# Kernel tuning notes

Measured on AMD Instinct MI355X. Metric: run time of the kernel, lower is better.

The kernel has to match this reference:

```python
import jax, jax.numpy as jnp
import numpy as np

D = 1024      # in_features
H = 4096      # hidden_dims
E = 8         # expert_nums
K = 2         # top_k
B, S = 4, 2048


def setup_inputs() -> dict:
    key = jax.random.key(0)
    ks = jax.random.split(key, 8)
    def lin(k, fan_in, shape):
        bound = 1.0 / np.sqrt(fan_in)
        return jax.random.uniform(k, shape, jnp.float32, -bound, bound)
    return {
        "x":  jax.random.normal(ks[0], (B, S, D), jnp.float32),
        "Wg": lin(ks[1], D, (D, E)),
        "bg": lin(ks[2], D, (E,)),
        "W1": lin(ks[3], D, (E, D, H)),
        "b1": lin(ks[4], D, (E, H)),
        "W2": lin(ks[5], H, (E, H, D)),
        "b2": lin(ks[6], H, (E, D)),
    }


def reference(x, Wg, bg, W1, b1, W2, b2):
    B_, S_, D_ = x.shape
    xt = x.reshape(-1, D_)                                   # [N, D]
    # Router: softmax gating + top-k
    logits = xt @ Wg + bg                                    # [N, E]
    scores = jax.nn.softmax(logits, axis=-1)
    topk_probs, topk_idx = jax.lax.top_k(scores, K)          # [N, K]
    # Dense per-expert FFN (the source runs every expert on all tokens)
    h = jnp.einsum("nd,edh->enh", xt, W1) + b1[:, None, :]   # [E, N, H]
    h = jax.nn.gelu(h, approximate=False)
    eo = jnp.einsum("enh,ehd->end", h, W2) + b2[:, None, :]  # [E, N, D]
    # Gather selected experts per token and combine with gate weights
    eo = jnp.transpose(eo, (1, 0, 2))                        # [N, E, D]
    sel = jnp.take_along_axis(eo, topk_idx[:, :, None], axis=1)  # [N, K, D]
    out = jnp.einsum("nk,nkd->nd", topk_probs, sel)          # [N, D]
    return out.reshape(B_, S_, D_)
```

## Files before the change

### kernel.cpp

```cpp
#include <hip/hip_runtime.h>
#include <hip/hip_bf16.h>
#include <cstdint>
#include <cstddef>

using bf16 = __hip_bfloat16;
using short8 = __attribute__((ext_vector_type(8))) short;
using floatx4 = __attribute__((ext_vector_type(4))) float;

constexpr int D_IN = 1024;
constexpr int H_DIM = 4096;
constexpr int E_NUM = 8;
constexpr int NTOK = 8192;
constexpr int NPAIR = NTOK * 2;

constexpr size_t OFF_PTOK  = 1024;
constexpr size_t OFF_PPROB = 263168;
constexpr size_t OFF_XBF   = 1048576;
constexpr size_t OFF_W2T   = OFF_XBF + (size_t)NTOK * D_IN * 2;
constexpr size_t OFF_HBUF  = OFF_W2T + (size_t)E_NUM * D_IN * H_DIM * 2;
constexpr size_t OFF_W1T   = OFF_HBUF + (size_t)NPAIR * H_DIM * 2;

__device__ __forceinline__ void cp16(const bf16* g, bf16* s) {
  __builtin_amdgcn_global_load_lds(
      (const __attribute__((address_space(1))) unsigned int*)g,
      (__attribute__((address_space(3))) unsigned int*)s, 16, 0, 0);
}

__global__ __launch_bounds__(256) void transpose_cvt(
    const float* __restrict__ in, bf16* __restrict__ out, int K, int N) {
  __shared__ float tile[32][33];
  const int e = blockIdx.z;
  const float* ip = in + (size_t)e * K * N + (size_t)(blockIdx.y * 32) * N + blockIdx.x * 32;
  bf16* op = out + (size_t)e * K * N + (size_t)(blockIdx.x * 32) * K + blockIdx.y * 32;
  const int tx = threadIdx.x & 31, ty = threadIdx.x >> 5;
#pragma unroll
  for (int r = 0; r < 4; r++)
    tile[ty + r * 8][tx] = ip[(size_t)(ty + r * 8) * N + tx];
  __syncthreads();
#pragma unroll
  for (int r = 0; r < 4; r++)
    op[(size_t)(ty + r * 8) * K + tx] = __float2bfloat16(tile[tx][ty + r * 8]);
}

__global__ __launch_bounds__(256) void router_kernel(
    const float* __restrict__ x, const float* __restrict__ Wg,
    const float* __restrict__ bg, bf16* __restrict__ Xbf,
    int* __restrict__ counts, int* __restrict__ pairTok, float* __restrict__ pairProb) {
  const int lane = threadIdx.x & 63;
  const int n = blockIdx.x * 4 + (threadIdx.x >> 6);
  const float* xr = x + (size_t)n * D_IN;
  bf16* xbr = Xbf + (size_t)n * D_IN;
  float logit[E_NUM];
#pragma unroll
  for (int e = 0; e < E_NUM; e++) logit[e] = 0.f;
#pragma unroll
  for (int i = 0; i < 16; i++) {
    const int d = i * 64 + lane;
    const float xd = xr[d];
    xbr[d] = __float2bfloat16(xd);
    const float4* wr = (const float4*)(Wg + (size_t)d * E_NUM);
    const float4 w0 = wr[0], w1 = wr[1];
    logit[0] += xd * w0.x; logit[1] += xd * w0.y;
    logit[2] += xd * w0.z; logit[3] += xd * w0.w;
    logit[4] += xd * w1.x; logit[5] += xd * w1.y;
    logit[6] += xd * w1.z; logit[7] += xd * w1.w;
  }
#pragma unroll
  for (int e = 0; e < E_NUM; e++) {
#pragma unroll
    for (int off = 32; off >= 1; off >>= 1)
      logit[e] += __shfl_xor(logit[e], off, 64);
  }
  if (lane == 0) {
    float l[E_NUM], mx = -1e30f;
#pragma unroll
    for (int e = 0; e < E_NUM; e++) { l[e] = logit[e] + bg[e]; mx = fmaxf(mx, l[e]); }
    float ex[E_NUM], s = 0.f;
#pragma unroll
    for (int e = 0; e < E_NUM; e++) { ex[e] = expf(l[e] - mx); s += ex[e]; }
    int i0 = 0;
#pragma unroll
    for (int e = 1; e < E_NUM; e++) if (l[e] > l[i0]) i0 = e;
    int i1 = (i0 == 0) ? 1 : 0;
#pragma unroll
    for (int e = 0; e < E_NUM; e++) if (e != i0 && l[e] > l[i1]) i1 = e;
    const float inv = 1.f / s;
    int pos = atomicAdd(&counts[i0], 1);
    pairTok[i0 * NTOK + pos] = n;
    pairProb[i0 * NTOK + pos] = ex[i0] * inv;
    pos = atomicAdd(&counts[i1], 1);
    pairTok[i1 * NTOK + pos] = n | (1 << 15);
    pairProb[i1 * NTOK + pos] = ex[i1] * inv;
  }
}

template <int MODE, int K, int NC>
__global__ __launch_bounds__(256) void gemm_kernel(
    const bf16* __restrict__ A, const bf16* __restrict__ Wt,
    const float* __restrict__ bias, const int* __restrict__ counts,
    const int* __restrict__ pairTok, const float* __restrict__ pairProb,
    bf16* __restrict__ Hout, float* __restrict__ Rout) {
  const int e = blockIdx.z;
  const int cnt = counts[e];
  const int m0 = blockIdx.y * 128;
  if (m0 >= cnt) return;
  const int n0 = blockIdx.x * 128;
  int base = 0;
  for (int i = 0; i < e; i++) base += counts[i];

  __shared__ __align__(16) bf16 As[128 * 32];
  __shared__ __align__(16) bf16 Bs[128 * 32];

  const int t = threadIdx.x;
  const int lane = t & 63;
  const int wave = t >> 6;
  const int wmq = wave >> 1, wnq = wave & 1;
  const int fr = lane & 15;
  const int kg = (lane >> 4) * 8;

  const bf16* aSrc[2];
  const bf16* bSrc[2];
#pragma unroll
  for (int i = 0; i < 2; i++) {
    const int lin = i * 256 + t;
    const int r = lin >> 2;
    const int c8 = (lin & 3) * 8;
    int p = m0 + r;
    if (p > cnt - 1) p = cnt - 1;
    if (MODE == 0) {
      const int tok = pairTok[e * NTOK + p] & 0x1FFF;
      aSrc[i] = A + (size_t)tok * K + c8;
    } else {
      aSrc[i] = A + (size_t)(base + p) * K + c8;
    }
    bSrc[i] = Wt + ((size_t)e * NC + n0 + r) * K + c8;
  }

  floatx4 acc[4][4];
#pragma unroll
  for (int ti = 0; ti < 4; ti++)
#pragma unroll
    for (int tj = 0; tj < 4; tj++)
      acc[ti][tj] = {0.f, 0.f, 0.f, 0.f};

  for (int k0 = 0; k0 < K; k0 += 32) {
#pragma unroll
    for (int i = 0; i < 2; i++) {
      cp16(aSrc[i] + k0, &As[(size_t)(i * 256 + t) * 8]);
      cp16(bSrc[i] + k0, &Bs[(size_t)(i * 256 + t) * 8]);
    }
    __syncthreads();
    short8 a[4], b[4];
#pragma unroll
    for (int ti = 0; ti < 4; ti++)
      a[ti] = *(const short8*)&As[(wmq * 64 + ti * 16 + fr) * 32 + kg];
#pragma unroll
    for (int tj = 0; tj < 4; tj++)
      b[tj] = *(const short8*)&Bs[(wnq * 64 + tj * 16 + fr) * 32 + kg];
#pragma unroll
    for (int ti = 0; ti < 4; ti++)
#pragma unroll
      for (int tj = 0; tj < 4; tj++)
        acc[ti][tj] = __builtin_amdgcn_mfma_f32_16x16x32_bf16(a[ti], b[tj], acc[ti][tj], 0, 0, 0);
    __syncthreads();
  }

  float bv[4];
#pragma unroll
  for (int tj = 0; tj < 4; tj++)
    bv[tj] = bias[(size_t)e * NC + n0 + wnq * 64 + tj * 16 + fr];

#pragma unroll
  for (int ti = 0; ti < 4; ti++) {
    const int rb = wmq * 64 + ti * 16 + (lane >> 4) * 4;
#pragma unroll
    for (int i = 0; i < 4; i++) {
      const int p = m0 + rb + i;
      if (p < cnt) {
        if (MODE == 0) {
          bf16* orow = Hout + (size_t)(base + p) * NC + n0 + wnq * 64 + fr;
#pragma unroll
          for (int tj = 0; tj < 4; tj++) {
            const float h = acc[ti][tj][i] + bv[tj];
            const float g = 0.5f * h * (1.f + erff(h * 0.70710678118f));
            orow[tj * 16] = __float2bfloat16(g);
          }
        } else {
          const int pt = pairTok[e * NTOK + p];
          const float pr = pairProb[e * NTOK + p];
          const int tok = pt & 0x1FFF, slot = (pt >> 15) & 1;
          float* orow = Rout + ((size_t)(tok * 2 + slot)) * NC + n0 + wnq * 64 + fr;
#pragma unroll
          for (int tj = 0; tj < 4; tj++)
            orow[tj * 16] = (acc[ti][tj][i] + bv[tj]) * pr;
        }
      }
    }
  }
}

__global__ __launch_bounds__(256) void combine_kernel(
    const float4* __restrict__ r, float4* __restrict__ o) {
  const int j = blockIdx.x * 256 + threadIdx.x;
  const int n = j >> 8, c = j & 255;
  const float4 a = r[(size_t)(n * 2) * 256 + c];
  const float4 b = r[(size_t)(n * 2 + 1) * 256 + c];
  o[j] = make_float4(a.x + b.x, a.y + b.y, a.z + b.z, a.w + b.w);
}

extern "C" void kernel_launch(void* const* d_in, const int* in_sizes, int n_in,
                              void* d_out, int out_size, void* d_ws, size_t ws_size,
                              hipStream_t stream) {
  const float* x  = (const float*)d_in[0];
  const float* Wg = (const float*)d_in[1];
  const float* bg = (const float*)d_in[2];
  const float* W1 = (const float*)d_in[3];
  const float* b1 = (const float*)d_in[4];
  const float* W2 = (const float*)d_in[5];
  const float* b2 = (const float*)d_in[6];
  float* out = (float*)d_out;
  char* ws = (char*)d_ws;

  int*   counts   = (int*)ws;
  int*   pairTok  = (int*)(ws + OFF_PTOK);
  float* pairProb = (float*)(ws + OFF_PPROB);
  bf16*  Xbf      = (bf16*)(ws + OFF_XBF);
  bf16*  W2t      = (bf16*)(ws + OFF_W2T);
  bf16*  Hbuf     = (bf16*)(ws + OFF_HBUF);
  bf16*  W1t      = (bf16*)(ws + OFF_W1T);
  float* resbuf   = (float*)W1t;

  hipMemsetAsync(counts, 0, 64, stream);
  transpose_cvt<<<dim3(H_DIM / 32, D_IN / 32, E_NUM), 256, 0, stream>>>(W1, W1t, D_IN, H_DIM);
  transpose_cvt<<<dim3(D_IN / 32, H_DIM / 32, E_NUM), 256, 0, stream>>>(W2, W2t, H_DIM, D_IN);
  router_kernel<<<NTOK / 4, 256, 0, stream>>>(x, Wg, bg, Xbf, counts, pairTok, pairProb);
  gemm_kernel<0, D_IN, H_DIM><<<dim3(H_DIM / 128, NTOK / 128, E_NUM), 256, 0, stream>>>(
      Xbf, W1t, b1, counts, pairTok, pairProb, Hbuf, resbuf);
  gemm_kernel<1, H_DIM, D_IN><<<dim3(D_IN / 128, NTOK / 128, E_NUM), 256, 0, stream>>>(
      Hbuf, W2t, b2, counts, pairTok, pairProb, Hbuf, resbuf);
  combine_kernel<<<(NTOK * D_IN / 4) / 256, 256, 0, stream>>>((const float4*)resbuf, (float4*)out);
}
```

Before: 988.8 us.

## Compact MoE GEMM tiles via schedule table and atomically combine expert outputs

Adds a single-thread scheduling kernel that builds a packed list of (expert, m-tile) pairs and per-expert base offsets. Both GEMMs now launch a 1D grid sized to at most 144 tiles, instead of a dense E x NTOK/128 grid where most blocks exit early. The second GEMM accumulates weighted results straight into the zeroed output with float atomicAdd, which removes the combine kernel and the fp32 intermediate buffer. In exchange it adds a serial scheduling launch, an output memset and atomic contention, and makes the fp32 summation order nondeterministic.

```diff
diff --git a/kernel.cpp b/kernel.cpp
--- a/kernel.cpp
+++ b/kernel.cpp
@@ -12,9 +12,11 @@
 constexpr int E_NUM = 8;
 constexpr int NTOK = 8192;
 constexpr int NPAIR = NTOK * 2;
+constexpr int MAXTILES = 144;
 
 constexpr size_t OFF_PTOK  = 1024;
 constexpr size_t OFF_PPROB = 263168;
+constexpr size_t OFF_SCHED = 525312;
 constexpr size_t OFF_XBF   = 1048576;
 constexpr size_t OFF_W2T   = OFF_XBF + (size_t)NTOK * D_IN * 2;
 constexpr size_t OFF_HBUF  = OFF_W2T + (size_t)E_NUM * D_IN * H_DIM * 2;
@@ -94,19 +96,37 @@
   }
 }
 
-template <int MODE, int K, int NC>
+__global__ void sched_kernel(const int* __restrict__ counts, int* __restrict__ sched) {
+  if (threadIdx.x == 0 && blockIdx.x == 0) {
+    int* bases = sched;
+    int* nTiles = sched + 8;
+    int* tileMap = sched + 16;
+    int base = 0, t = 0;
+    for (int e = 0; e < E_NUM; e++) {
+      bases[e] = base;
+      const int nt = (counts[e] + 127) >> 7;
+      for (int m = 0; m < nt; m++) tileMap[t++] = (e << 16) | m;
+      base += counts[e];
+    }
+    *nTiles = t;
+  }
+}
+
+template <int MODE, int K, int NC, int NTX>
 __global__ __launch_bounds__(256) void gemm_kernel(
     const bf16* __restrict__ A, const bf16* __restrict__ Wt,
     const float* __restrict__ bias, const int* __restrict__ counts,
     const int* __restrict__ pairTok, const float* __restrict__ pairProb,
-    bf16* __restrict__ Hout, float* __restrict__ Rout) {
-  const int e = blockIdx.z;
+    const int* __restrict__ sched, bf16* __restrict__ Hout, float* __restrict__ Out) {
+  const int nblk = blockIdx.x % NTX;
+  const int tix = blockIdx.x / NTX;
+  if (tix >= sched[8]) return;
+  const int packed = sched[16 + tix];
+  const int e = packed >> 16;
+  const int m0 = (packed & 0xFFFF) * 128;
   const int cnt = counts[e];
-  const int m0 = blockIdx.y * 128;
-  if (m0 >= cnt) return;
-  const int n0 = blockIdx.x * 128;
-  int base = 0;
-  for (int i = 0; i < e; i++) base += counts[i];
+  const int base = sched[e];
+  const int n0 = nblk * 128;
 
   __shared__ __align__(16) bf16 As[128 * 32];
   __shared__ __align__(16) bf16 Bs[128 * 32];
@@ -188,24 +208,15 @@
         } else {
           const int pt = pairTok[e * NTOK + p];
           const float pr = pairProb[e * NTOK + p];
-          const int tok = pt & 0x1FFF, slot = (pt >> 15) & 1;
-          float* orow = Rout + ((size_t)(tok * 2 + slot)) * NC + n0 + wnq * 64 + fr;
+          const int tok = pt & 0x1FFF;
+          float* orow = Out + (size_t)tok * NC + n0 + wnq * 64 + fr;
 #pragma unroll
           for (int tj = 0; tj < 4; tj++)
-            orow[tj * 16] = (acc[ti][tj][i] + bv[tj]) * pr;
+            atomicAdd(&orow[tj * 16], (acc[ti][tj][i] + bv[tj]) * pr);
         }
       }
     }
   }
-}
-
-__global__ __launch_bounds__(256) void combine_kernel(
-    const float4* __restrict__ r, float4* __restrict__ o) {
-  const int j = blockIdx.x * 256 + threadIdx.x;
-  const int n = j >> 8, c = j & 255;
-  const float4 a = r[(size_t)(n * 2) * 256 + c];
-  const float4 b = r[(size_t)(n * 2 + 1) * 256 + c];
-  o[j] = make_float4(a.x + b.x, a.y + b.y, a.z + b.z, a.w + b.w);
 }
 
 extern "C" void kernel_launch(void* const* d_in, const int* in_sizes, int n_in,
@@ -224,19 +235,20 @@
   int*   counts   = (int*)ws;
   int*   pairTok  = (int*)(ws + OFF_PTOK);
   float* pairProb = (float*)(ws + OFF_PPROB);
+  int*   sched    = (int*)(ws + OFF_SCHED);
   bf16*  Xbf      = (bf16*)(ws + OFF_XBF);
   bf16*  W2t      = (bf16*)(ws + OFF_W2T);
   bf16*  Hbuf     = (bf16*)(ws + OFF_HBUF);
   bf16*  W1t      = (bf16*)(ws + OFF_W1T);
-  float* resbuf   = (float*)W1t;
 
   hipMemsetAsync(counts, 0, 64, stream);
+  hipMemsetAsync(out, 0, (size_t)out_size * sizeof(float), stream);
   transpose_cvt<<<dim3(H_DIM / 32, D_IN / 32, E_NUM), 256, 0, stream>>>(W1, W1t, D_IN, H_DIM);
   transpose_cvt<<<dim3(D_IN / 32, H_DIM / 32, E_NUM), 256, 0, stream>>>(W2, W2t, H_DIM, D_IN);
   router_kernel<<<NTOK / 4, 256, 0, stream>>>(x, Wg, bg, Xbf, counts, pairTok, pairProb);
-  gemm_kernel<0, D_IN, H_DIM><<<dim3(H_DIM / 128, NTOK / 128, E_NUM), 256, 0, stream>>>(
-      Xbf, W1t, b1, counts, pairTok, pairProb, Hbuf, resbuf);
-  gemm_kernel<1, H_DIM, D_IN><<<dim3(D_IN / 128, NTOK / 128, E_NUM), 256, 0, stream>>>(
-      Hbuf, W2t, b2, counts, pairTok, pairProb, Hbuf, resbuf);
-  combine_kernel<<<(NTOK * D_IN / 4) / 256, 256, 0, stream>>>((const float4*)resbuf, (float4*)out);
-}
+  sched_kernel<<<1, 64, 0, stream>>>(counts, sched);
+  gemm_kernel<0, D_IN, H_DIM, 32><<<32 * MAXTILES, 256, 0, stream>>>(
+      Xbf, W1t, b1, counts, pairTok, pairProb, sched, Hbuf, out);
+  gemm_kernel<1, H_DIM, D_IN, 8><<<8 * MAXTILES, 256, 0, stream>>>(
+      Hbuf, W2t, b2, counts, pairTok, pairProb, sched, Hbuf, out);
+}
```

Result: slower. 1.013 ms (+2.4%).
